# Kernel tuning notes

Measured on AMD Instinct MI355X. Metric: run time of the kernel, lower is better.

The kernel has to match this reference:

```python
import jax, jax.numpy as jnp
import numpy as np

MARGIN = 0.5
B, D, P = 4096, 4096, 8


def setup_inputs() -> dict:
    key = jax.random.key(0)
    kx, kp = jax.random.split(key)
    x = jax.random.normal(kx, (B, D), dtype=jnp.float32)
    pos_ids = jax.random.randint(kp, (B, P), 0, D, dtype=jnp.int64)
    # y is the multi-hot label vector consistent with pos_ids: y[i, k] = 1 for k in pos_ids[i]
    y = jnp.zeros((B, D), dtype=jnp.float32)
    y = y.at[jnp.arange(B)[:, None], pos_ids].set(1.0)
    return {"x": x, "y": y, "pos_ids": pos_ids}


def reference(x, y, pos_ids):
    # x: [B, D] scores, y: [B, D] multi-hot labels, pos_ids: [B, P] positive indices
    x_pos = jnp.take_along_axis(x, pos_ids, axis=1)              # [B, P] anchor scores x[i, k]
    # margin violations: relu(margin + x[i, d] - x[i, k]) for every (k, d) pair
    viol = jnp.maximum(0.0, MARGIN + x[:, None, :] - x_pos[:, :, None])  # [B, P, D]
    # (1 - y[i]) masks out positive classes from the negative side
    loss = jnp.sum((1.0 - y)[:, None, :] * viol)
    count = B * P * (D - P)  # original: sum_i sum_{k in pos_ids[i]} (D - len(pos_ids[i]))
    return loss / count
```

## Files before the change

kernel.cpp:

```cpp
#include <hip/hip_runtime.h>
#include <hip/hip_bf16.h>

#define MB 4096
#define MD 4096
#define MP 8
#define MARGIN 0.5f

typedef float f32x4 __attribute__((ext_vector_type(4)));

__global__ __launch_bounds__(256) void margin_rows_kernel(
    const float* __restrict__ x,
    const int* __restrict__ pos_ids,
    float* __restrict__ ws)
{
    const int row = blockIdx.x;
    const int t = threadIdx.x;
    const int lane = t & 63;
    const int wave = t >> 6;
    const float* __restrict__ xr = x + (size_t)row * MD;

    const int p = pos_ids[row * MP + (lane & 7)];

    const f32x4* __restrict__ xr4 = reinterpret_cast<const f32x4*>(xr);
    const f32x4 v0 = __builtin_nontemporal_load(xr4 + t);
    const f32x4 v1 = __builtin_nontemporal_load(xr4 + 256 + t);
    const f32x4 v2 = __builtin_nontemporal_load(xr4 + 512 + t);
    const f32x4 v3 = __builtin_nontemporal_load(xr4 + 768 + t);

    const float xg = xr[p];

    float th[MP];
    int   pi[MP];
#pragma unroll
    for (int k = 0; k < MP; ++k) {
        th[k] = __shfl(xg, k, 64) - MARGIN;
        pi[k] = __shfl(p, k, 64);
    }

    const float vv[16] = { v0.x, v0.y, v0.z, v0.w,
                           v1.x, v1.y, v1.z, v1.w,
                           v2.x, v2.y, v2.z, v2.w,
                           v3.x, v3.y, v3.z, v3.w };

    float acc0 = 0.0f, acc1 = 0.0f;
#pragma unroll
    for (int j = 0; j < 16; ++j) {
        const float v = vv[j];
#pragma unroll
        for (int k = 0; k < MP; k += 2) {
            acc0 += fmaxf(0.0f, v - th[k]);
            acc1 += fmaxf(0.0f, v - th[k + 1]);
        }
    }

    if (t < MP) {
        bool dup = false;
#pragma unroll
        for (int k2 = 0; k2 < MP; ++k2) dup = dup || (k2 < t && pi[k2] == pi[t]);
        if (!dup) {
            const float xk = th[t] + MARGIN;
#pragma unroll
            for (int j = 0; j < MP; ++j)
                acc0 -= fmaxf(0.0f, xk - th[j]);
        }
    }

    float acc = acc0 + acc1;
#pragma unroll
    for (int off = 32; off > 0; off >>= 1)
        acc += __shfl_down(acc, off, 64);

    __shared__ float s_part[4];
    if (lane == 0) s_part[wave] = acc;
    __syncthreads();
    if (t == 0)
        ws[row] = s_part[0] + s_part[1] + s_part[2] + s_part[3];
}

__global__ __launch_bounds__(256) void margin_final_kernel(
    const float* __restrict__ ws,
    float* __restrict__ out)
{
    const int t = threadIdx.x;
    double acc = 0.0;
#pragma unroll
    for (int it = 0; it < MB / 256; ++it)
        acc += (double)ws[it * 256 + t];

#pragma unroll
    for (int off = 32; off > 0; off >>= 1)
        acc += __shfl_down(acc, off, 64);

    __shared__ double s_part[4];
    const int wave = t >> 6;
    if ((t & 63) == 0) s_part[wave] = acc;
    __syncthreads();
    if (t == 0) {
        const double tot = s_part[0] + s_part[1] + s_part[2] + s_part[3];
        const double count = (double)MB * (double)MP * (double)(MD - MP);
        out[0] = (float)(tot / count);
    }
}

extern "C" void kernel_launch(void* const* d_in, const int* in_sizes, int n_in,
                              void* d_out, int out_size, void* d_ws, size_t ws_size,
                              hipStream_t stream) {
    const float* x = (const float*)d_in[0];
    const int* pos_ids = (const int*)d_in[2];
    float* out = (float*)d_out;
    float* ws = (float*)d_ws;

    margin_rows_kernel<<<MB, 256, 0, stream>>>(x, pos_ids, ws);
    margin_final_kernel<<<1, 256, 0, stream>>>(ws, out);
}
```

Measured before the change: 18.81 us.

## Process two rows per block and rewrite hinge as max minus threshold

Each block now handles two rows, with all eight vector loads issued up front so more memory traffic is in flight per thread, and the grid shrinks to half as many blocks. The hinge relu(v - th) is rewritten as max(v, th) - th, with the threshold sums subtracted once per row, which removes one subtract per element pair. Duplicate detection now uses shuffles instead of a precomputed index array. The cost is higher register pressure and fewer blocks to spread across the CUs, and the algebraic rewrite may change float rounding slightly.

```diff
diff --git a/kernel.cpp b/kernel.cpp
--- a/kernel.cpp
+++ b/kernel.cpp
@@ -5,6 +5,8 @@
 #define MD 4096
 #define MP 8
 #define MARGIN 0.5f
+#define RPB 2
+#define NBLK (MB / RPB)
 
 typedef float f32x4 __attribute__((ext_vector_type(4)));
 
@@ -13,55 +15,104 @@
     const int* __restrict__ pos_ids,
     float* __restrict__ ws)
 {
-    const int row = blockIdx.x;
+    const int row0 = blockIdx.x * RPB;
     const int t = threadIdx.x;
     const int lane = t & 63;
     const int wave = t >> 6;
-    const float* __restrict__ xr = x + (size_t)row * MD;
+    const float* __restrict__ xr0 = x + (size_t)row0 * MD;
+    const float* __restrict__ xr1 = xr0 + MD;
 
-    const int p = pos_ids[row * MP + (lane & 7)];
+    const int p0 = pos_ids[row0 * MP + (lane & 7)];
+    const int p1 = pos_ids[row0 * MP + MP + (lane & 7)];
 
-    const f32x4* __restrict__ xr4 = reinterpret_cast<const f32x4*>(xr);
-    const f32x4 v0 = __builtin_nontemporal_load(xr4 + t);
-    const f32x4 v1 = __builtin_nontemporal_load(xr4 + 256 + t);
-    const f32x4 v2 = __builtin_nontemporal_load(xr4 + 512 + t);
-    const f32x4 v3 = __builtin_nontemporal_load(xr4 + 768 + t);
+    const f32x4* __restrict__ x40 = reinterpret_cast<const f32x4*>(xr0);
+    const f32x4* __restrict__ x41 = reinterpret_cast<const f32x4*>(xr1);
+    const f32x4 a0 = __builtin_nontemporal_load(x40 + t);
+    const f32x4 a1 = __builtin_nontemporal_load(x40 + 256 + t);
+    const f32x4 a2 = __builtin_nontemporal_load(x40 + 512 + t);
+    const f32x4 a3 = __builtin_nontemporal_load(x40 + 768 + t);
+    const f32x4 b0 = __builtin_nontemporal_load(x41 + t);
+    const f32x4 b1 = __builtin_nontemporal_load(x41 + 256 + t);
+    const f32x4 b2 = __builtin_nontemporal_load(x41 + 512 + t);
+    const f32x4 b3 = __builtin_nontemporal_load(x41 + 768 + t);
 
-    const float xg = xr[p];
+    const float xg0 = xr0[p0];
+    const float xg1 = xr1[p1];
 
-    float th[MP];
-    int   pi[MP];
+    float th0[MP];
 #pragma unroll
-    for (int k = 0; k < MP; ++k) {
-        th[k] = __shfl(xg, k, 64) - MARGIN;
-        pi[k] = __shfl(p, k, 64);
+    for (int k = 0; k < MP; ++k) th0[k] = __shfl(xg0, k, 64) - MARGIN;
+    float sum_th0 = 0.0f;
+#pragma unroll
+    for (int k = 0; k < MP; ++k) sum_th0 += th0[k];
+
+    float acc0 = 0.0f, acc1 = 0.0f;
+
+    {
+        const float vv[16] = { a0.x, a0.y, a0.z, a0.w,
+                               a1.x, a1.y, a1.z, a1.w,
+                               a2.x, a2.y, a2.z, a2.w,
+                               a3.x, a3.y, a3.z, a3.w };
+#pragma unroll
+        for (int j = 0; j < 16; ++j) {
+            const float v = vv[j];
+#pragma unroll
+            for (int k = 0; k < MP; k += 2) {
+                acc0 += fmaxf(v, th0[k]);
+                acc1 += fmaxf(v, th0[k + 1]);
+            }
+        }
+        acc0 -= 16.0f * sum_th0;
     }
 
-    const float vv[16] = { v0.x, v0.y, v0.z, v0.w,
-                           v1.x, v1.y, v1.z, v1.w,
-                           v2.x, v2.y, v2.z, v2.w,
-                           v3.x, v3.y, v3.z, v3.w };
+    float th1[MP];
+#pragma unroll
+    for (int k = 0; k < MP; ++k) th1[k] = __shfl(xg1, k, 64) - MARGIN;
+    float sum_th1 = 0.0f;
+#pragma unroll
+    for (int k = 0; k < MP; ++k) sum_th1 += th1[k];
 
-    float acc0 = 0.0f, acc1 = 0.0f;
+    {
+        const float vv[16] = { b0.x, b0.y, b0.z, b0.w,
+                               b1.x, b1.y, b1.z, b1.w,
+                               b2.x, b2.y, b2.z, b2.w,
+                               b3.x, b3.y, b3.z, b3.w };
 #pragma unroll
-    for (int j = 0; j < 16; ++j) {
-        const float v = vv[j];
+        for (int j = 0; j < 16; ++j) {
+            const float v = vv[j];
 #pragma unroll
-        for (int k = 0; k < MP; k += 2) {
-            acc0 += fmaxf(0.0f, v - th[k]);
-            acc1 += fmaxf(0.0f, v - th[k + 1]);
+            for (int k = 0; k < MP; k += 2) {
+                acc0 += fmaxf(v, th1[k]);
+                acc1 += fmaxf(v, th1[k + 1]);
+            }
         }
+        acc0 -= 16.0f * sum_th1;
     }
 
     if (t < MP) {
+        const int myp = __shfl(p0, t, 64);
         bool dup = false;
 #pragma unroll
-        for (int k2 = 0; k2 < MP; ++k2) dup = dup || (k2 < t && pi[k2] == pi[t]);
+        for (int k2 = 0; k2 < MP; ++k2)
+            dup = dup || (k2 < t && __shfl(p0, k2, 64) == myp);
         if (!dup) {
-            const float xk = th[t] + MARGIN;
+            const float xk = th0[t] + MARGIN;
 #pragma unroll
             for (int j = 0; j < MP; ++j)
-                acc0 -= fmaxf(0.0f, xk - th[j]);
+                acc0 -= fmaxf(0.0f, xk - th0[j]);
+        }
+    } else if (t < 2 * MP) {
+        const int i = t - MP;
+        const int myp = __shfl(p1, i, 64);
+        bool dup = false;
+#pragma unroll
+        for (int k2 = 0; k2 < MP; ++k2)
+            dup = dup || (k2 < i && __shfl(p1, k2, 64) == myp);
+        if (!dup) {
+            const float xk = th1[i] + MARGIN;
+#pragma unroll
+            for (int j = 0; j < MP; ++j)
+                acc0 -= fmaxf(0.0f, xk - th1[j]);
         }
     }
 
@@ -74,7 +125,7 @@
     if (lane == 0) s_part[wave] = acc;
     __syncthreads();
     if (t == 0)
-        ws[row] = s_part[0] + s_part[1] + s_part[2] + s_part[3];
+        ws[blockIdx.x] = s_part[0] + s_part[1] + s_part[2] + s_part[3];
 }
 
 __global__ __launch_bounds__(256) void margin_final_kernel(
@@ -84,7 +135,7 @@
     const int t = threadIdx.x;
     double acc = 0.0;
 #pragma unroll
-    for (int it = 0; it < MB / 256; ++it)
+    for (int it = 0; it < NBLK / 256; ++it)
         acc += (double)ws[it * 256 + t];
 
 #pragma unroll
@@ -110,6 +161,6 @@
     float* out = (float*)d_out;
     float* ws = (float*)d_ws;
 
-    margin_rows_kernel<<<MB, 256, 0, stream>>>(x, pos_ids, ws);
+    margin_rows_kernel<<<NBLK, 256, 0, stream>>>(x, pos_ids, ws);
     margin_final_kernel<<<1, 256, 0, stream>>>(ws, out);
 }
```

Measured after the change: 18.94 us. About the same (+0.7%).
